# Performance work log

Measured on AMD Instinct MI355X. Metric: run time of the kernel, lower is better.

## Reference

```python
import jax, jax.numpy as jnp
import numpy as np

B, S, MODEL_DIM = 4, 512, 128
FEAT = 2 * MODEL_DIM  # hidden feature dim must be 2*model_dim for Ws


def setup_inputs() -> dict:
    key = jax.random.key(0)
    k1, k2, k3 = jax.random.split(key, 3)
    hidden = jax.random.normal(k1, (B, S, FEAT), dtype=jnp.float32)
    # nn.Linear(2*model_dim, model_dim, bias=False): weight [model_dim, 2*model_dim]
    Ws = jax.random.normal(k2, (MODEL_DIM, FEAT), dtype=jnp.float32) * (1.0 / np.sqrt(FEAT))
    # nn.Linear(model_dim, 1, bias=False): weight [1, model_dim]
    vs = jax.random.normal(k3, (1, MODEL_DIM), dtype=jnp.float32) * (1.0 / np.sqrt(MODEL_DIM))
    return {"hidden": hidden, "Ws": Ws, "vs": vs}


def reference(hidden, Ws, vs):
    # query*key broadcast: [B, S, S, 2D]
    prod = hidden[:, None, :, :] * hidden[:, :, None, :]
    # MLP score: Linear -> tanh -> Linear, squeeze -> [B, S, S]
    h = jnp.tanh(jnp.einsum('bqkf,df->bqkd', prod, Ws))
    sjt = jnp.einsum('bqkd,d->bqk', h, vs[0])
    atten = jax.nn.softmax(sjt, axis=2)  # dropout = identity (eval)
    context = jnp.einsum('bqk,bkf->bqf', atten, hidden)
    return (context, atten)
```

## Files before the change

### kernel.cpp

```cpp
#include <hip/hip_runtime.h>
#include <hip/hip_bf16.h>

#define Bb 4
#define Ss 512
#define Ff 256
#define Dd 128

typedef __attribute__((ext_vector_type(8))) short bf8_t;
typedef __attribute__((ext_vector_type(4))) float f32x4;

__device__ __forceinline__ short bfbits(float x) {
  union { __hip_bfloat16 b; short s; } u;
  u.b = __hip_bfloat16(x);
  return u.s;
}

__device__ __forceinline__ float fast_tanh(float x) {
  float e = exp2f(x * 2.8853900818f);
  return 1.0f - 2.0f * __builtin_amdgcn_rcpf(e + 1.0f);
}

typedef __attribute__((address_space(3))) unsigned int lds_u32;
typedef const __attribute__((address_space(1))) unsigned int glb_u32;
__device__ __forceinline__ void load_lds16(const void* g, void* l) {
  __builtin_amdgcn_global_load_lds((glb_u32*)g, (lds_u32*)l, 16, 0, 0);
}

__global__ __launch_bounds__(256) void cvt_kernel(const float* __restrict__ hidden,
                                                  short* __restrict__ hbf) {
  const int idx = blockIdx.x * 256 + threadIdx.x;
  const int lin = idx * 4;
  const float4 v = *(const float4*)(hidden + lin);
  const int r = lin >> 8;
  const int c = lin & 255;
  const int cs = c ^ ((r & 7) << 3);
  short4 o = make_short4(bfbits(v.x), bfbits(v.y), bfbits(v.z), bfbits(v.w));
  *(short4*)(hbf + ((size_t)r << 8) + cs) = o;
}

__global__ __launch_bounds__(256) void score_kernel(
    const float* __restrict__ hidden, const short* __restrict__ hbf,
    const float* __restrict__ Ws, const float* __restrict__ vs,
    float* __restrict__ Sws)
{
  __shared__ __align__(16) short htile[4][2][16 * 256];
  __shared__ float s_full[2][512];

  const int tid   = threadIdx.x;
  const int lane  = tid & 63;
  const int w     = tid >> 6;
  const int col16 = lane & 15;
  const int grp   = lane >> 4;

  const int blk  = blockIdx.x;
  const int b    = blk & 3;
  const int pair = blk >> 2;
  const int q0   = pair * 2;
  const int kstart = q0 & ~15;
  const int nkf  = (Ss - kstart) >> 4;

  const float* Hb  = hidden + (size_t)b * Ss * Ff;
  const short* hsb = hbf + (size_t)b * Ss * Ff;
  float*       Sb  = Sws + (size_t)b * Ss * Ss;

  bf8_t afr[2][2][8];
  #pragma unroll
  for (int ks = 0; ks < 8; ++ks) {
    const int f0 = ks * 32 + grp * 8;
    float4 h0[2], h1[2];
    #pragma unroll
    for (int g = 0; g < 2; ++g) {
      const float* hq = Hb + (size_t)(q0 + g) * Ff + f0;
      h0[g] = *(const float4*)(hq);
      h1[g] = *(const float4*)(hq + 4);
    }
    #pragma unroll
    for (int mf = 0; mf < 2; ++mf) {
      const int d = w * 32 + mf * 16 + col16;
      const float* wr = Ws + (size_t)d * Ff + f0;
      const float4 w0 = *(const float4*)(wr);
      const float4 w1 = *(const float4*)(wr + 4);
      #pragma unroll
      for (int g = 0; g < 2; ++g) {
        bf8_t t;
        t[0] = bfbits(h0[g].x * w0.x); t[1] = bfbits(h0[g].y * w0.y);
        t[2] = bfbits(h0[g].z * w0.z); t[3] = bfbits(h0[g].w * w0.w);
        t[4] = bfbits(h1[g].x * w1.x); t[5] = bfbits(h1[g].y * w1.y);
        t[6] = bfbits(h1[g].z * w1.z); t[7] = bfbits(h1[g].w * w1.w);
        afr[g][mf][ks] = t;
      }
    }
  }

  float m2v[2][4];
  float base = 0.f;
  #pragma unroll
  for (int mf = 0; mf < 2; ++mf)
    #pragma unroll
    for (int r = 0; r < 4; ++r) {
      const float v = vs[w * 32 + mf * 16 + grp * 4 + r];
      m2v[mf][r] = -2.0f * v;
      base += v;
    }

  {
    float* sf = (float*)s_full;
    sf[tid] = 0.f; sf[tid + 256] = 0.f; sf[tid + 512] = 0.f; sf[tid + 768] = 0.f;
  }
  __syncthreads();

  {
    const short* src = hsb + (size_t)kstart * Ff;
    short* dst = &htile[w][0][0];
    #pragma unroll
    for (int seg = 0; seg < 8; ++seg)
      load_lds16(src + seg * 512 + lane * 8, dst + seg * 512);
  }

  const int swz = (col16 & 7) << 3;
  const int rbase = col16 * 256;

  int cur = 0;
  for (int i = 0; i < nkf; ++i) {
    const int k16 = kstart + i * 16;
    if (i + 1 < nkf) {
      const short* src = hsb + (size_t)(k16 + 16) * Ff;
      short* dst = &htile[w][cur ^ 1][0];
      #pragma unroll
      for (int seg = 0; seg < 8; ++seg)
        load_lds16(src + seg * 512 + lane * 8, dst + seg * 512);
      asm volatile("s_waitcnt vmcnt(8)" ::: "memory");
    } else {
      asm volatile("s_waitcnt vmcnt(0)" ::: "memory");
    }
    __builtin_amdgcn_sched_barrier(0);

    const short* bufp = &htile[w][cur][0];
    f32x4 acc[2][2] = {};
    #pragma unroll
    for (int ks = 0; ks < 8; ++ks) {
      const int coff = (ks * 32 + grp * 8) ^ swz;
      const bf8_t bbv = *(const bf8_t*)(bufp + rbase + coff);
      acc[0][0] = __builtin_amdgcn_mfma_f32_16x16x32_bf16(afr[0][0][ks], bbv, acc[0][0], 0, 0, 0);
      acc[0][1] = __builtin_amdgcn_mfma_f32_16x16x32_bf16(afr[0][1][ks], bbv, acc[0][1], 0, 0, 0);
      acc[1][0] = __builtin_amdgcn_mfma_f32_16x16x32_bf16(afr[1][0][ks], bbv, acc[1][0], 0, 0, 0);
      acc[1][1] = __builtin_amdgcn_mfma_f32_16x16x32_bf16(afr[1][1][ks], bbv, acc[1][1], 0, 0, 0);
    }
    #pragma unroll
    for (int g = 0; g < 2; ++g) {
      float ps = base;
      #pragma unroll
      for (int mf = 0; mf < 2; ++mf)
        #pragma unroll
        for (int r = 0; r < 4; ++r) {
          const float e = exp2f(acc[g][mf][r] * 2.8853900818f);
          ps += m2v[mf][r] * __builtin_amdgcn_rcpf(e + 1.0f);
        }
      ps += __shfl_xor(ps, 16);
      ps += __shfl_xor(ps, 32);
      if (lane < 16)
        atomicAdd(&s_full[g][k16 + lane], ps);
    }
    cur ^= 1;
  }
  __syncthreads();

  for (int k = q0 + tid; k < Ss; k += 256)
    Sb[(size_t)q0 * Ss + k] = s_full[0][k];
  for (int k = q0 + tid; k < Ss; k += 256)
    Sb[(size_t)(q0 + 1) * Ss + k] = s_full[1][k];
  for (int k = q0 + 2 + tid; k < Ss; k += 256) {
    const float2 v = make_float2(s_full[0][k], s_full[1][k]);
    *(float2*)(&Sb[(size_t)k * Ss + q0]) = v;
  }
}

__global__ __launch_bounds__(256) void ctx_kernel(
    const float* __restrict__ hidden, const float* __restrict__ Sws,
    float* __restrict__ out)
{
  __shared__ float p[4][512];
  __shared__ float ctxp[4][4][256];

  const int tid = threadIdx.x, lane = tid & 63, w = tid >> 6;
  const int blk = blockIdx.x;
  const int b   = blk >> 7;
  const int q0  = (blk & 127) * 4;

  const float* Sb = Sws + (size_t)b * Ss * Ss;
  const float* Hb = hidden + (size_t)b * Ss * Ff;

  {
    const int q = q0 + w;
    const float* Srow = Sb + (size_t)q * Ss;
    const float4 x0 = *(const float4*)(Srow + lane * 8);
    const float4 x1 = *(const float4*)(Srow + lane * 8 + 4);
    float m = fmaxf(fmaxf(fmaxf(x0.x, x0.y), fmaxf(x0.z, x0.w)),
                    fmaxf(fmaxf(x1.x, x1.y), fmaxf(x1.z, x1.w)));
    #pragma unroll
    for (int d = 1; d < 64; d <<= 1) m = fmaxf(m, __shfl_xor(m, d));
    float4 e0, e1;
    e0.x = exp2f((x0.x - m) * 1.44269504f); e0.y = exp2f((x0.y - m) * 1.44269504f);
    e0.z = exp2f((x0.z - m) * 1.44269504f); e0.w = exp2f((x0.w - m) * 1.44269504f);
    e1.x = exp2f((x1.x - m) * 1.44269504f); e1.y = exp2f((x1.y - m) * 1.44269504f);
    e1.z = exp2f((x1.z - m) * 1.44269504f); e1.w = exp2f((x1.w - m) * 1.44269504f);
    float sm = e0.x + e0.y + e0.z + e0.w + e1.x + e1.y + e1.z + e1.w;
    #pragma unroll
    for (int d = 1; d < 64; d <<= 1) sm += __shfl_xor(sm, d);
    const float inv = 1.0f / sm;
    e0.x *= inv; e0.y *= inv; e0.z *= inv; e0.w *= inv;
    e1.x *= inv; e1.y *= inv; e1.z *= inv; e1.w *= inv;
    float* att = out + (size_t)Bb * Ss * Ff + ((size_t)(b * Ss + q)) * Ss;
    *(float4*)(att + lane * 8)     = e0;
    *(float4*)(att + lane * 8 + 4) = e1;
    *(float4*)(&p[w][lane * 8])     = e0;
    *(float4*)(&p[w][lane * 8 + 4]) = e1;
  }
  __syncthreads();

  float4 cg[4] = {{0,0,0,0},{0,0,0,0},{0,0,0,0},{0,0,0,0}};
  const float* hp = Hb + (size_t)(w * 128) * Ff + lane * 4;
  #pragma unroll 4
  for (int k = 0; k < 128; ++k) {
    const float4 h = *(const float4*)(hp + (size_t)k * Ff);
    #pragma unroll
    for (int g = 0; g < 4; ++g) {
      const float a = p[g][w * 128 + k];
      cg[g].x += a * h.x; cg[g].y += a * h.y; cg[g].z += a * h.z; cg[g].w += a * h.w;
    }
  }
  #pragma unroll
  for (int g = 0; g < 4; ++g)
    *(float4*)(&ctxp[w][g][lane * 4]) = cg[g];
  __syncthreads();
  #pragma unroll
  for (int rep = 0; rep < 4; ++rep) {
    const int idx = rep * 256 + tid;
    const int g = idx >> 8, f = idx & 255;
    out[((size_t)(b * Ss) + q0 + g) * Ff + f] =
        ctxp[0][g][f] + ctxp[1][g][f] + ctxp[2][g][f] + ctxp[3][g][f];
  }
}

__global__ __launch_bounds__(256) void selfatten_fallback(
    const float* __restrict__ hidden, const float* __restrict__ Ws,
    const float* __restrict__ vs, float* __restrict__ out)
{
  __shared__ __align__(16) short htile[2][64][264];
  __shared__ float s_part[2][4][2][64];
  __shared__ float s_full[2][512];
  __shared__ float red[8];

  const int tid = threadIdx.x, lane = tid & 63, w = tid >> 6;
  const int col16 = lane & 15, grp = lane >> 4;
  const int blk = blockIdx.x, b = blk >> 8, q0 = (blk & 255) * 2;
  const float* Hb = hidden + (size_t)b * Ss * Ff;

  bf8_t afr[2][2][8];
  #pragma unroll
  for (int ks = 0; ks < 8; ++ks) {
    const int f0 = ks * 32 + grp * 8;
    #pragma unroll
    for (int mf = 0; mf < 2; ++mf) {
      const int d = w * 32 + mf * 16 + col16;
      const float* wr = Ws + (size_t)d * Ff + f0;
      const float4 w0 = *(const float4*)(wr);
      const float4 w1 = *(const float4*)(wr + 4);
      #pragma unroll
      for (int g = 0; g < 2; ++g) {
        const float* hq = Hb + (size_t)(q0 + g) * Ff + f0;
        const float4 h0 = *(const float4*)(hq);
        const float4 h1 = *(const float4*)(hq + 4);
        bf8_t t;
        t[0] = bfbits(h0.x * w0.x); t[1] = bfbits(h0.y * w0.y);
        t[2] = bfbits(h0.z * w0.z); t[3] = bfbits(h0.w * w0.w);
        t[4] = bfbits(h1.x * w1.x); t[5] = bfbits(h1.y * w1.y);
        t[6] = bfbits(h1.z * w1.z); t[7] = bfbits(h1.w * w1.w);
        afr[g][mf][ks] = t;
      }
    }
  }
  float vsv[2][4];
  #pragma unroll
  for (int mf = 0; mf < 2; ++mf)
    #pragma unroll
    for (int r = 0; r < 4; ++r) vsv[mf][r] = vs[w * 32 + mf * 16 + grp * 4 + r];

  #pragma unroll
  for (int it = 0; it < 8; ++it) {
    const int lin = it * 2048 + tid * 8;
    const float4 v0 = *(const float4*)(Hb + lin);
    const float4 v1 = *(const float4*)(Hb + lin + 4);
    const int row = lin >> 8, col = lin & 255;
    bf8_t o;
    o[0] = bfbits(v0.x); o[1] = bfbits(v0.y); o[2] = bfbits(v0.z); o[3] = bfbits(v0.w);
    o[4] = bfbits(v1.x); o[5] = bfbits(v1.y); o[6] = bfbits(v1.z); o[7] = bfbits(v1.w);
    *(bf8_t*)(&htile[0][row][col]) = o;
  }
  __syncthreads();
  int cur = 0;
  for (int c = 0; c < 8; ++c) {
    const int k0 = c * 64, nxt = cur ^ 1, cb = c & 1;
    const float* src = Hb + (size_t)(k0 + 64) * Ff;
    #pragma unroll
    for (int nf = 0; nf < 4; ++nf) {
      float4 sv[4];
      if (c < 7) {
        #pragma unroll
        for (int i = 0; i < 2; ++i) {
          const int lin = (nf * 2 + i) * 2048 + tid * 8;
          sv[2 * i] = *(const float4*)(src + lin);
          sv[2 * i + 1] = *(const float4*)(src + lin + 4);
        }
      }
      f32x4 acc[2][2] = {};
      #pragma unroll
      for (int ks = 0; ks < 8; ++ks) {
        const bf8_t bbv = *(const bf8_t*)(&htile[cur][nf * 16 + col16][ks * 32 + grp * 8]);
        #pragma unroll
        for (int g = 0; g < 2; ++g) {
          acc[g][0] = __builtin_amdgcn_mfma_f32_16x16x32_bf16(afr[g][0][ks], bbv, acc[g][0], 0, 0, 0);
          acc[g][1] = __builtin_amdgcn_mfma_f32_16x16x32_bf16(afr[g][1][ks], bbv, acc[g][1], 0, 0, 0);
        }
      }
      #pragma unroll
      for (int g = 0; g < 2; ++g) {
        float ps = 0.f;
        #pragma unroll
        for (int mf = 0; mf < 2; ++mf)
          #pragma unroll
          for (int r = 0; r < 4; ++r) ps += vsv[mf][r] * fast_tanh(acc[g][mf][r]);
        ps += __shfl_xor(ps, 16);
        ps += __shfl_xor(ps, 32);
        if (lane < 16) s_part[cb][w][g][nf * 16 + lane] = ps;
      }
      if (c < 7) {
        #pragma unroll
        for (int i = 0; i < 2; ++i) {
          const int lin = (nf * 2 + i) * 2048 + tid * 8;
          const int row = lin >> 8, col = lin & 255;
          const float4 a = sv[2 * i], bsv = sv[2 * i + 1];
          bf8_t o;
          o[0] = bfbits(a.x); o[1] = bfbits(a.y); o[2] = bfbits(a.z); o[3] = bfbits(a.w);
          o[4] = bfbits(bsv.x); o[5] = bfbits(bsv.y); o[6] = bfbits(bsv.z); o[7] = bfbits(bsv.w);
          *(bf8_t*)(&htile[nxt][row][col]) = o;
        }
      }
    }
    __syncthreads();
    if (tid < 128) {
      const int g = tid >> 6, key = tid & 63;
      s_full[g][k0 + key] = s_part[cb][0][g][key] + s_part[cb][1][g][key] +
                            s_part[cb][2][g][key] + s_part[cb][3][g][key];
    }
    cur = nxt;
  }
  __syncthreads();
  float av[2][2];
  #pragma unroll
  for (int g = 0; g < 2; ++g) {
    const float s0 = s_full[g][tid], s1 = s_full[g][tid + 256];
    float m = fmaxf(s0, s1);
    #pragma unroll
    for (int d = 1; d < 64; d <<= 1) m = fmaxf(m, __shfl_xor(m, d));
    if (lane == 0) red[w] = m;
    __syncthreads();
    m = fmaxf(fmaxf(red[0], red[1]), fmaxf(red[2], red[3]));
    const float p0 = exp2f((s0 - m) * 1.44269504f);
    const float p1 = exp2f((s1 - m) * 1.44269504f);
    float sm = p0 + p1;
    #pragma unroll
    for (int d = 1; d < 64; d <<= 1) sm += __shfl_xor(sm, d);
    if (lane == 0) red[4 + w] = sm;
    __syncthreads();
    const float inv = 1.0f / (red[4] + red[5] + red[6] + red[7]);
    av[g][0] = p0 * inv; av[g][1] = p1 * inv;
    float* attp = out + (size_t)Bb * Ss * Ff + ((size_t)(b * Ss + q0 + g)) * Ss;
    attp[tid] = av[g][0];
    attp[tid + 256] = av[g][1];
    __syncthreads();
  }
  s_full[0][tid] = av[0][0]; s_full[0][tid + 256] = av[0][1];
  s_full[1][tid] = av[1][0]; s_full[1][tid + 256] = av[1][1];
  __syncthreads();
  float* ctxp = (float*)htile;
  float4 c0v = {0,0,0,0}, c1v = {0,0,0,0};
  const float* hp = Hb + (size_t)(w * 128) * Ff + lane * 4;
  #pragma unroll 8
  for (int k = 0; k < 128; ++k) {
    const float4 h = *(const float4*)(hp + (size_t)k * Ff);
    const float a0 = s_full[0][w * 128 + k];
    const float a1 = s_full[1][w * 128 + k];
    c0v.x += a0 * h.x; c0v.y += a0 * h.y; c0v.z += a0 * h.z; c0v.w += a0 * h.w;
    c1v.x += a1 * h.x; c1v.y += a1 * h.y; c1v.z += a1 * h.z; c1v.w += a1 * h.w;
  }
  *(float4*)(&ctxp[(w * 2 + 0) * 256 + lane * 4]) = c0v;
  *(float4*)(&ctxp[(w * 2 + 1) * 256 + lane * 4]) = c1v;
  __syncthreads();
  #pragma unroll
  for (int rep = 0; rep < 2; ++rep) {
    const int idx = tid + rep * 256;
    const int g = idx >> 8, f = idx & 255;
    out[((size_t)(b * Ss) + q0 + g) * Ff + f] =
        ctxp[(0 * 2 + g) * 256 + f] + ctxp[(1 * 2 + g) * 256 + f] +
        ctxp[(2 * 2 + g) * 256 + f] + ctxp[(3 * 2 + g) * 256 + f];
  }
}

extern "C" void kernel_launch(void* const* d_in, const int* in_sizes, int n_in,
                              void* d_out, int out_size, void* d_ws, size_t ws_size,
                              hipStream_t stream) {
  (void)in_sizes; (void)n_in; (void)out_size;
  const float* hidden = (const float*)d_in[0];
  const float* Ws     = (const float*)d_in[1];
  const float* vs     = (const float*)d_in[2];
  float* out          = (float*)d_out;

  const size_t hbf_bytes = (size_t)Bb * Ss * Ff * sizeof(short);
  const size_t sws_bytes = (size_t)Bb * Ss * Ss * sizeof(float);
  if (ws_size >= hbf_bytes + sws_bytes) {
    short* hbf = (short*)d_ws;
    float* Sws = (float*)((char*)d_ws + hbf_bytes);
    cvt_kernel<<<dim3(Bb * Ss * Ff / 4 / 256), dim3(256), 0, stream>>>(hidden, hbf);
    score_kernel<<<dim3(Bb * Ss / 2), dim3(256), 0, stream>>>(hidden, hbf, Ws, vs, Sws);
    ctx_kernel<<<dim3(Bb * Ss / 4), dim3(256), 0, stream>>>(hidden, Sws, out);
  } else {
    selfatten_fallback<<<dim3(Bb * Ss / 2), dim3(256), 0, stream>>>(hidden, Ws, vs, out);
  }
}
```

Baseline: 95.26 us.

## Share 64-row key tiles across waves in score kernel with block-wide double buffering

Before, each wave loaded its own private copy of every 16-row key tile into LDS. Now a single 64-row key chunk is loaded cooperatively by all four waves into a shared double buffer, and each wave computes four 16-row fragments from it. The first chunk's prefetch is issued before the A-fragment setup so its latency overlaps that work. This cuts redundant global-to-LDS traffic fourfold, at the cost of a block-wide __syncthreads per chunk and coarser 64-row start alignment, which wastes some work on the causal-like triangle.

```diff
diff --git a/kernel.cpp b/kernel.cpp
--- a/kernel.cpp
+++ b/kernel.cpp
@@ -43,7 +43,7 @@
     const float* __restrict__ Ws, const float* __restrict__ vs,
     float* __restrict__ Sws)
 {
-  __shared__ __align__(16) short htile[4][2][16 * 256];
+  __shared__ __align__(16) short htile[2][64 * 256];
   __shared__ float s_full[2][512];
 
   const int tid   = threadIdx.x;
@@ -56,12 +56,20 @@
   const int b    = blk & 3;
   const int pair = blk >> 2;
   const int q0   = pair * 2;
-  const int kstart = q0 & ~15;
-  const int nkf  = (Ss - kstart) >> 4;
+  const int c0   = q0 >> 6;
 
   const float* Hb  = hidden + (size_t)b * Ss * Ff;
   const short* hsb = hbf + (size_t)b * Ss * Ff;
   float*       Sb  = Sws + (size_t)b * Ss * Ss;
+
+  {
+    const short* src = hsb + (size_t)c0 * (64 * 256);
+    #pragma unroll
+    for (int i = 0; i < 8; ++i) {
+      const int seg = i * 4 + w;
+      load_lds16(src + seg * 512 + lane * 8, &htile[0][seg * 512]);
+    }
+  }
 
   bf8_t afr[2][2][8];
   #pragma unroll
@@ -107,59 +115,51 @@
     float* sf = (float*)s_full;
     sf[tid] = 0.f; sf[tid + 256] = 0.f; sf[tid + 512] = 0.f; sf[tid + 768] = 0.f;
   }
-  __syncthreads();
-
-  {
-    const short* src = hsb + (size_t)kstart * Ff;
-    short* dst = &htile[w][0][0];
-    #pragma unroll
-    for (int seg = 0; seg < 8; ++seg)
-      load_lds16(src + seg * 512 + lane * 8, dst + seg * 512);
-  }
 
   const int swz = (col16 & 7) << 3;
-  const int rbase = col16 * 256;
 
   int cur = 0;
-  for (int i = 0; i < nkf; ++i) {
-    const int k16 = kstart + i * 16;
-    if (i + 1 < nkf) {
-      const short* src = hsb + (size_t)(k16 + 16) * Ff;
-      short* dst = &htile[w][cur ^ 1][0];
-      #pragma unroll
-      for (int seg = 0; seg < 8; ++seg)
-        load_lds16(src + seg * 512 + lane * 8, dst + seg * 512);
-      asm volatile("s_waitcnt vmcnt(8)" ::: "memory");
-    } else {
-      asm volatile("s_waitcnt vmcnt(0)" ::: "memory");
-    }
-    __builtin_amdgcn_sched_barrier(0);
-
-    const short* bufp = &htile[w][cur][0];
-    f32x4 acc[2][2] = {};
-    #pragma unroll
-    for (int ks = 0; ks < 8; ++ks) {
-      const int coff = (ks * 32 + grp * 8) ^ swz;
-      const bf8_t bbv = *(const bf8_t*)(bufp + rbase + coff);
-      acc[0][0] = __builtin_amdgcn_mfma_f32_16x16x32_bf16(afr[0][0][ks], bbv, acc[0][0], 0, 0, 0);
-      acc[0][1] = __builtin_amdgcn_mfma_f32_16x16x32_bf16(afr[0][1][ks], bbv, acc[0][1], 0, 0, 0);
-      acc[1][0] = __builtin_amdgcn_mfma_f32_16x16x32_bf16(afr[1][0][ks], bbv, acc[1][0], 0, 0, 0);
-      acc[1][1] = __builtin_amdgcn_mfma_f32_16x16x32_bf16(afr[1][1][ks], bbv, acc[1][1], 0, 0, 0);
-    }
-    #pragma unroll
-    for (int g = 0; g < 2; ++g) {
-      float ps = base;
-      #pragma unroll
-      for (int mf = 0; mf < 2; ++mf)
+  for (int c = c0; c < 8; ++c) {
+    const int k0 = c << 6;
+    __syncthreads();
+    if (c < 7) {
+      const short* src = hsb + (size_t)(c + 1) * (64 * 256);
+      const int nb = cur ^ 1;
+      #pragma unroll
+      for (int i = 0; i < 8; ++i) {
+        const int seg = i * 4 + w;
+        load_lds16(src + seg * 512 + lane * 8, &htile[nb][seg * 512]);
+      }
+    }
+
+    #pragma unroll
+    for (int nf = 0; nf < 4; ++nf) {
+      f32x4 acc[2][2] = {};
+      const int rbase = nf * 4096 + col16 * 256;
+      #pragma unroll
+      for (int ks = 0; ks < 8; ++ks) {
+        const int coff = (ks * 32 + grp * 8) ^ swz;
+        const bf8_t bbv = *(const bf8_t*)(&htile[cur][rbase + coff]);
+        acc[0][0] = __builtin_amdgcn_mfma_f32_16x16x32_bf16(afr[0][0][ks], bbv, acc[0][0], 0, 0, 0);
+        acc[0][1] = __builtin_amdgcn_mfma_f32_16x16x32_bf16(afr[0][1][ks], bbv, acc[0][1], 0, 0, 0);
+        acc[1][0] = __builtin_amdgcn_mfma_f32_16x16x32_bf16(afr[1][0][ks], bbv, acc[1][0], 0, 0, 0);
+        acc[1][1] = __builtin_amdgcn_mfma_f32_16x16x32_bf16(afr[1][1][ks], bbv, acc[1][1], 0, 0, 0);
+      }
+      #pragma unroll
+      for (int g = 0; g < 2; ++g) {
+        float ps = base;
         #pragma unroll
-        for (int r = 0; r < 4; ++r) {
-          const float e = exp2f(acc[g][mf][r] * 2.8853900818f);
-          ps += m2v[mf][r] * __builtin_amdgcn_rcpf(e + 1.0f);
-        }
-      ps += __shfl_xor(ps, 16);
-      ps += __shfl_xor(ps, 32);
-      if (lane < 16)
-        atomicAdd(&s_full[g][k16 + lane], ps);
+        for (int mf = 0; mf < 2; ++mf)
+          #pragma unroll
+          for (int r = 0; r < 4; ++r) {
+            const float e = exp2f(acc[g][mf][r] * 2.8853900818f);
+            ps += m2v[mf][r] * __builtin_amdgcn_rcpf(e + 1.0f);
+          }
+        ps += __shfl_xor(ps, 16);
+        ps += __shfl_xor(ps, 32);
+        if (lane < 16)
+          atomicAdd(&s_full[g][k0 + nf * 16 + lane], ps);
+      }
     }
     cur ^= 1;
   }
```

Measured after the change: 87.65 us. 8.0% less time.
